# Kernel optimization log

Hardware: AMD Instinct MI355X
Metric: run time of the kernel (lower is better)

## Reference

```python
import jax, jax.numpy as jnp
import numpy as np

N = 50           # hardcoded num_nodes in the module
E = 400          # directed edges (200 undirected)
D = 5            # node feature dim after laplacian concat
NEG_SLOPE = 0.2  # GATConv leaky_relu slope


def _edge_softmax(logits, seg, n):
    # softmax over edges grouped by target node (PyG softmax semantics)
    m = jax.ops.segment_max(logits, seg, num_segments=n)
    e = jnp.exp(logits - m[seg])
    s = jax.ops.segment_sum(e, seg, num_segments=n)
    return e / (s[seg] + 1e-16)


def _laplacian_evecs(edge_index, k=2):
    # sym-normalized Laplacian L = I - D^{-1/2} A D^{-1/2}, dense (N=50)
    src, dst = edge_index[0], edge_index[1]
    A = jnp.zeros((N, N), jnp.float32).at[src, dst].add(1.0)
    deg = A.sum(1)
    dis = jnp.where(deg > 0, jax.lax.rsqrt(jnp.maximum(deg, 1e-12)), 0.0)
    L = jnp.eye(N, dtype=jnp.float32) - dis[:, None] * A * dis[None, :]
    evals, evecs = jnp.linalg.eigh(L)  # ascending, like torch.linalg.eigh
    return evecs[:, :k], evals[1]


def _gat_conv(x, src, dst, w, a_src, a_dst, b):
    h = x @ w.T                                       # [N, out]
    e = jax.nn.leaky_relu((h * a_src).sum(-1)[src] + (h * a_dst).sum(-1)[dst], NEG_SLOPE)
    alpha = _edge_softmax(e, dst, N)
    out = jax.ops.segment_sum(alpha[:, None] * h[src], dst, num_segments=N)
    return out + b


def _transformer_conv(x, src, dst, wq, bq, wk, bk, wv, bv, ws, bs):
    q = x @ wq.T + bq
    k = x @ wk.T + bk
    v = x @ wv.T + bv
    alpha = _edge_softmax((q[dst] * k[src]).sum(-1) / jnp.sqrt(jnp.float32(D)), dst, N)
    out = jax.ops.segment_sum(alpha[:, None] * v[src], dst, num_segments=N)
    return out + x @ ws.T + bs    # root skip connection


def _core(x, mask, gat_w1, gat_a_src1, gat_a_dst1, gat_b1,
          gat_w2, gat_a_src2, gat_a_dst2, gat_b2,
          mha_in_w, mha_in_b, mha_out_w, mha_out_b,
          tc_wq, tc_bq, tc_wk, tc_bk, tc_wv, tc_bv, tc_ws, tc_bs,
          mlp_w1, mlp_b1, mlp_w2, mlp_b2, critic_w, critic_b,
          edge_index, lap_ev):
    x_combined = jnp.concatenate([x, lap_ev], axis=1)        # [N, 5]
    sl = jnp.arange(N, dtype=edge_index.dtype)
    ei = jnp.concatenate([edge_index, jnp.stack([sl, sl])], axis=1)  # add_self_loops
    src, dst = ei[0], ei[1]
    # GAT: 2 GATConv layers, ReLU between (BasicGNN), no act on last
    h = jax.nn.relu(_gat_conv(x_combined, src, dst, gat_w1, gat_a_src1, gat_a_dst1, gat_b1))
    h = _gat_conv(h, src, dst, gat_w2, gat_a_src2, gat_a_dst2, gat_b2)   # [N, 5]
    # nn.MultiheadAttention, seq=N, batch=1, 1 head
    qkv = h @ mha_in_w.T + mha_in_b
    q, k, v = jnp.split(qkv, 3, axis=1)
    attn = jax.nn.softmax(q @ k.T / jnp.sqrt(jnp.float32(D)), axis=-1)   # [N, N]
    h = (attn @ v) @ mha_out_w.T + mha_out_b
    # TransformerConv(5, 5, heads=1)
    h = _transformer_conv(h, src, dst, tc_wq, tc_bq, tc_wk, tc_bk, tc_wv, tc_bv, tc_ws, tc_bs)
    # MLPAggregation with index=arange(N): each node alone in a graph, slot 0 of N
    flat = jnp.pad(h, ((0, 0), (0, D * N - D)))              # [N, 5N]
    logits = jax.nn.relu(flat @ mlp_w1.T + mlp_b1) @ mlp_w2.T + mlp_b2   # [N, N]
    masked_logits = logits * mask[None, :]
    value = (logits @ critic_w.T + critic_b).mean()
    return masked_logits, value, x_combined, ei


def setup_inputs() -> dict:
    key = jax.random.key(0)
    ks = jax.random.split(key, 40)
    # symmetric edge list without self loops (networkx undirected -> both directions)
    row = jax.random.randint(ks[0], (E // 2,), 0, N)
    off = jax.random.randint(ks[1], (E // 2,), 1, N)
    col = (row + off) % N
    edge_index = jnp.concatenate([jnp.stack([row, col]), jnp.stack([col, row])], axis=1).astype(jnp.int32)
    lin = lambda k, o, i: (jax.random.normal(k, (o, i), jnp.float32) / np.sqrt(i))
    vec = lambda k, o: jax.random.normal(k, (o,), jnp.float32) * 0.1
    return {
        'x': jax.random.uniform(ks[2], (N, 3), jnp.float32),
        'edge_index': edge_index,
        'mask': (jax.random.uniform(ks[3], (N,)) > 0.2).astype(jnp.float32),
        'gat_w1': lin(ks[4], 8, 5), 'gat_a_src1': vec(ks[5], 8), 'gat_a_dst1': vec(ks[6], 8), 'gat_b1': vec(ks[7], 8),
        'gat_w2': lin(ks[8], 5, 8), 'gat_a_src2': vec(ks[9], 5), 'gat_a_dst2': vec(ks[10], 5), 'gat_b2': vec(ks[11], 5),
        'mha_in_w': lin(ks[12], 15, 5), 'mha_in_b': vec(ks[13], 15),
        'mha_out_w': lin(ks[14], 5, 5), 'mha_out_b': vec(ks[15], 5),
        'tc_wq': lin(ks[16], 5, 5), 'tc_bq': vec(ks[17], 5),
        'tc_wk': lin(ks[18], 5, 5), 'tc_bk': vec(ks[19], 5),
        'tc_wv': lin(ks[20], 5, 5), 'tc_bv': vec(ks[21], 5),
        'tc_ws': lin(ks[22], 5, 5), 'tc_bs': vec(ks[23], 5),
        'mlp_w1': lin(ks[24], 64, D * N), 'mlp_b1': vec(ks[25], 64),
        'mlp_w2': lin(ks[26], N, 64), 'mlp_b2': vec(ks[27], N),
        'critic_w': lin(ks[28], 1, N), 'critic_b': vec(ks[29], 1),
    }


def reference(x, edge_index, mask, gat_w1, gat_a_src1, gat_a_dst1, gat_b1,
              gat_w2, gat_a_src2, gat_a_dst2, gat_b2,
              mha_in_w, mha_in_b, mha_out_w, mha_out_b,
              tc_wq, tc_bq, tc_wk, tc_bk, tc_wv, tc_bv, tc_ws, tc_bs,
              mlp_w1, mlp_b1, mlp_w2, mlp_b2, critic_w, critic_b):
    lap_ev, _fiedler = _laplacian_evecs(edge_index)
    return _core(x, mask, gat_w1, gat_a_src1, gat_a_dst1, gat_b1,
                 gat_w2, gat_a_src2, gat_a_dst2, gat_b2,
                 mha_in_w, mha_in_b, mha_out_w, mha_out_b,
                 tc_wq, tc_bq, tc_wk, tc_bk, tc_wv, tc_bv, tc_ws, tc_bs,
                 mlp_w1, mlp_b1, mlp_w2, mlp_b2, critic_w, critic_b,
                 edge_index, lap_ev)
```

## Files before the change

### kernel.cpp

```cpp
#include <hip/hip_runtime.h>
#include <math.h>

#define NN 50
#define E2 400
#define ET 450
#define NTHR 256
#define KL 8
#define QS 52
#define MS 68

#define WSYNC() do { asm volatile("s_waitcnt lgkmcnt(0)" ::: "memory"); \
                     __builtin_amdgcn_sched_barrier(0); } while (0)

__global__ __launch_bounds__(NTHR, 1) void opn_kernel(
    const float* __restrict__ gx, const int* __restrict__ gedge,
    const float* __restrict__ gmask,
    const float* __restrict__ w1, const float* __restrict__ as1,
    const float* __restrict__ ad1, const float* __restrict__ b1,
    const float* __restrict__ w2, const float* __restrict__ as2,
    const float* __restrict__ ad2, const float* __restrict__ b2,
    const float* __restrict__ miw, const float* __restrict__ mib,
    const float* __restrict__ mow, const float* __restrict__ mob,
    const float* __restrict__ wq, const float* __restrict__ bq,
    const float* __restrict__ wk, const float* __restrict__ bk,
    const float* __restrict__ wv, const float* __restrict__ bv,
    const float* __restrict__ ws, const float* __restrict__ bs,
    const float* __restrict__ mw1, const float* __restrict__ mb1,
    const float* __restrict__ mw2, const float* __restrict__ mb2,
    const float* __restrict__ cw, const float* __restrict__ cb,
    float* __restrict__ out)
{
    const int tid = threadIdx.x;

    __shared__ float sM[NN * NN];
    __shared__ alignas(16) float sS[3200];
    __shared__ alignas(16) float sL[NN * QS];
    __shared__ alignas(16) float sQ2[(KL + 2) * QS];
    __shared__ float sAl_[KL + 2];
    __shared__ float sBe_[KL + 2];
    __shared__ float sY[KL + 2];
    __shared__ float sCp[KL + 2];
    __shared__ float sDp2[KL + 2];
    __shared__ int   sKeff;
    __shared__ float sB5h[NN * 5];
    __shared__ float sKv[NN * 5];
    __shared__ float sVv[NN * 5];
    __shared__ float sTk[NN * 5];
    __shared__ float sTv[NN * 5];
    __shared__ float sTo[NN * 5];
    __shared__ int   sSrc[ET];
    __shared__ int   sDst[ET];
    __shared__ int   sSrcCsr[ET];
    __shared__ float sAs[NN];
    __shared__ float sAsB[NN];
    __shared__ float sdis[NN];
    __shared__ float sred[4];
    __shared__ int   sOff[NN + 1];
    __shared__ float sW1[40], sAs1[8], sAd1[8], sB1[8];
    __shared__ float sW2[40], sAs2[5], sAd2[5], sB2[5];
    __shared__ float sMiw[75], sMib[15], sMow[25], sMob[5];
    __shared__ float sWq[25], sBq[5], sWk[25], sBk[5];
    __shared__ float sWv[25], sBv[5], sWsk[25], sBsk[5];
    __shared__ float sMw1[320], sMb1[64];
    __shared__ alignas(16) float sMw2[NN * MS];
    __shared__ float sMb2[NN], sCw[NN], sCb0[1], sMask[NN];

    const float inv_sqrt5 = 0.4472135954999579f;
    float xr0 = 0, xr1 = 0, xr2 = 0, xr3 = 0, xr4 = 0;

    if (tid < 64) {
        const int lane = tid;
        {
            int gi = (lane < NN) ? lane : NN - 1;
            xr0 = gx[gi * 3 + 0]; xr1 = gx[gi * 3 + 1]; xr2 = gx[gi * 3 + 2];
        }
        int es[7], ed[7];
#pragma unroll
        for (int u = 0; u < 7; ++u) {
            int e = lane + u * 64;
            int ec = (e < E2) ? e : E2 - 1;
            es[u] = gedge[ec]; ed[u] = gedge[E2 + ec];
        }
        if (lane == 0) sKeff = KL;
        for (int t = lane; t < NN * NN; t += 64) sM[t] = 0.0f;
        WSYNC();
#pragma unroll
        for (int u = 0; u < 7; ++u) {
            int e = lane + u * 64;
            if (e < E2) atomicAdd(&sM[es[u] * NN + ed[u]], 1.0f);
        }
        WSYNC();
        float dsum = 0.0f;
        if (lane < NN) {
            const float* rp = &sM[lane * NN];
            for (int k = 0; k < NN; ++k) dsum += rp[k];
        }
        float disl = (dsum > 0.0f) ? (1.0f / sqrtf(fmaxf(dsum, 1e-12f))) : 0.0f;
        if (lane < NN) sdis[lane] = disl;
        WSYNC();
        for (int t = lane; t < NN * QS; t += 64) {
            int i = t / QS, k = t - i * QS;
            sL[t] = (k < NN)
                  ? (((i == k) ? 1.0f : 0.0f) - sdis[i] * sM[i * NN + k] * sdis[k])
                  : 0.0f;
        }
        float q0r, qprev = 0.0f, qcur;
        {
            float q0 = (lane < NN) ? sqrtf(dsum) : 0.0f;
            float nn = q0 * q0;
            for (int off = 32; off > 0; off >>= 1) nn += __shfl_xor(nn, off);
            q0 *= rsqrtf(nn);
            unsigned u = (unsigned)lane * 2654435761u + 12345u;
            u ^= u >> 13; u *= 2246822519u; u ^= u >> 11;
            float q1 = (lane < NN) ? ((float)(u & 0xFFFF) * (1.0f / 65536.0f) - 0.5f) : 0.0f;
            for (int pass = 0; pass < 2; ++pass) {
                float d = q0 * q1;
                for (int off = 32; off > 0; off >>= 1) d += __shfl_xor(d, off);
                q1 -= d * q0;
            }
            float n1 = q1 * q1;
            for (int off = 32; off > 0; off >>= 1) n1 += __shfl_xor(n1, off);
            q1 *= rsqrtf(n1);
            q0r = q0; qcur = q1;
            if (lane < NN) { sQ2[lane] = q0; sQ2[QS + lane] = q1; }
            WSYNC();
        }
        for (int j = 1; j <= KL; ++j) {
            const float* qp = &sQ2[j * QS];
            const float4* qp4 = (const float4*)qp;
            float w = 0.0f;
            if (lane < NN) {
                const float* rp = &sL[lane * QS];
                const float4* rp4 = (const float4*)rp;
                float a0 = 0.0f, a1 = 0.0f, a2 = 0.0f, a3 = 0.0f;
                for (int k = 0; k < 12; ++k) {
                    float4 r = rp4[k], q = qp4[k];
                    a0 += r.x * q.x; a1 += r.y * q.y;
                    a2 += r.z * q.z; a3 += r.w * q.w;
                }
                a0 += rp[48] * qp[48];
                a1 += rp[49] * qp[49];
                w = 2.0f * qcur - (a0 + a1 + a2 + a3);
            }
            float c0 = q0r * w, c1 = qprev * w, ca = qcur * w;
#pragma unroll
            for (int off = 32; off > 0; off >>= 1) {
                c0 += __shfl_xor(c0, off);
                c1 += __shfl_xor(c1, off);
                ca += __shfl_xor(ca, off);
            }
            w -= c0 * q0r + c1 * qprev + ca * qcur;
            float nn2 = w * w;
#pragma unroll
            for (int off = 32; off > 0; off >>= 1) nn2 += __shfl_xor(nn2, off);
            float beta = sqrtf(nn2);
            if (lane == 0) { sAl_[j] = ca; sBe_[j] = beta; }
            if (j < KL) {
                if (beta > 1e-10f) {
                    qprev = qcur;
                    qcur = w * (1.0f / beta);
                    if (lane < NN) sQ2[(j + 1) * QS + lane] = qcur;
                    WSYNC();
                } else {
                    if (lane == 0) sKeff = j;
                    break;
                }
            }
        }
        WSYNC();
        const int keff = sKeff;
        float lo = 1e30f, hi = -1e30f;
        for (int m = 1; m <= keff; ++m) {
            float r = ((m > 1) ? fabsf(sBe_[m - 1]) : 0.0f)
                    + ((m < keff) ? fabsf(sBe_[m]) : 0.0f);
            lo = fminf(lo, sAl_[m] - r);
            hi = fmaxf(hi, sAl_[m] + r);
        }
        for (int round = 0; round < 4; ++round) {
            float h = (hi - lo) * (1.0f / 65.0f);
            float x = lo + (float)(lane + 1) * h;
            int cnt = 0;
            float d = sAl_[1] - x;
            if (d < 0.0f) cnt++;
            for (int m = 2; m <= keff; ++m) {
                float b = sBe_[m - 1];
                float dd = (fabsf(d) < 1e-20f) ? ((d >= 0.0f) ? 1e-20f : -1e-20f) : d;
                d = sAl_[m] - x - b * b / dd;
                if (d < 0.0f) cnt++;
            }
            unsigned long long msk = __ballot(cnt >= keff);
            int f = (msk == 0ULL) ? 64 : (__ffsll((unsigned long long)msk) - 1);
            float nlo = (f == 0) ? lo : (lo + (float)f * h);
            float nhi = (f == 64) ? hi : (lo + (float)(f + 1) * h);
            lo = nlo; hi = nhi;
        }
        const float th = 0.5f * (lo + hi);
        if (lane == 0) {
            if (keff == 1) {
                sY[1] = 1.0f;
            } else {
                float inv0 = rsqrtf((float)keff);
                for (int m = 1; m <= keff; ++m) sY[m] = inv0;
                float d1 = sAl_[1] - th;
                if (fabsf(d1) < 1e-10f) d1 = (d1 >= 0.0f) ? 1e-10f : -1e-10f;
                sCp[1] = sBe_[1] / d1;
                sDp2[1] = sY[1] / d1;
                for (int m = 2; m <= keff; ++m) {
                    float den = sAl_[m] - th - sBe_[m - 1] * sCp[m - 1];
                    if (fabsf(den) < 1e-10f) den = (den >= 0.0f) ? 1e-10f : -1e-10f;
                    if (m < keff) sCp[m] = sBe_[m] / den;
                    sDp2[m] = (sY[m] - sBe_[m - 1] * sDp2[m - 1]) / den;
                }
                sY[keff] = sDp2[keff];
                for (int m = keff - 1; m >= 1; --m)
                    sY[m] = sDp2[m] - sCp[m] * sY[m + 1];
                float nn = 0.0f;
                for (int m = 1; m <= keff; ++m) nn += sY[m] * sY[m];
                float sc = rsqrtf(nn);
                for (int m = 1; m <= keff; ++m) sY[m] *= sc;
            }
        }
        WSYNC();
        float v = 0.0f;
        if (lane < NN)
            for (int m = 1; m <= keff; ++m) v += sY[m] * sQ2[m * QS + lane];
        {
            float nn = v * v;
            for (int off = 32; off > 0; off >>= 1) nn += __shfl_xor(nn, off);
            float av = fabsf(v);
            for (int off = 32; off > 0; off >>= 1) av = fmaxf(av, __shfl_xor(av, off));
            unsigned long long msk = __ballot((fabsf(v) == av) && (lane < NN));
            int fl = __ffsll((unsigned long long)msk) - 1;
            float sv = __shfl(v, fl);
            v *= ((sv >= 0.0f) ? 1.0f : -1.0f) * rsqrtf(nn);
        }
        xr3 = q0r; xr4 = v;
        if (lane < NN) {
            out[2501 + lane * 5 + 0] = xr0;
            out[2501 + lane * 5 + 1] = xr1;
            out[2501 + lane * 5 + 2] = xr2;
            out[2501 + lane * 5 + 3] = xr3;
            out[2501 + lane * 5 + 4] = xr4;
        }
    } else if (tid < 128) {
        const int l = tid - 64;
        for (int t = l; t < ET; t += 64) {
            int s, d;
            if (t < E2) { s = gedge[t]; d = gedge[E2 + t]; }
            else        { s = t - E2;   d = t - E2; }
            sSrc[t] = s; sDst[t] = d;
        }
        WSYNC();
        int cnt = 0;
        if (l < NN)
            for (int e = 0; e < ET; ++e) cnt += (sDst[e] == l) ? 1 : 0;
        int inc = cnt;
#pragma unroll
        for (int off = 1; off < 64; off <<= 1) {
            int n = __shfl_up(inc, off);
            if (l >= off) inc += n;
        }
        int exc = inc - cnt;
        if (l < NN) sOff[l] = exc;
        if (l == NN - 1) sOff[NN] = inc;
        if (l < NN) {
            int pos = exc;
            for (int e = 0; e < ET; ++e)
                if (sDst[e] == l) { sSrcCsr[pos] = sSrc[e]; ++pos; }
        }
        for (int t = l; t < 2 * ET; t += 64) {
            int val = (t < ET) ? sSrc[t] : sDst[t - ET];
            out[2751 + t] = (float)val;
        }
    } else {
        const int t0 = tid - 128;
        float vW1  = w1 [t0 < 40 ? t0 : 39];
        float vAs1 = as1[t0 < 8  ? t0 : 7];
        float vAd1 = ad1[t0 < 8  ? t0 : 7];
        float vB1  = b1 [t0 < 8  ? t0 : 7];
        float vW2  = w2 [t0 < 40 ? t0 : 39];
        float vAs2 = as2[t0 < 5  ? t0 : 4];
        float vAd2 = ad2[t0 < 5  ? t0 : 4];
        float vB2  = b2 [t0 < 5  ? t0 : 4];
        float vMiw = miw[t0 < 75 ? t0 : 74];
        float vMib = mib[t0 < 15 ? t0 : 14];
        float vMow = mow[t0 < 25 ? t0 : 24];
        float vMob = mob[t0 < 5  ? t0 : 4];
        float vWq  = wq [t0 < 25 ? t0 : 24];
        float vBq  = bq [t0 < 5  ? t0 : 4];
        float vWk  = wk [t0 < 25 ? t0 : 24];
        float vBk  = bk [t0 < 5  ? t0 : 4];
        float vWv  = wv [t0 < 25 ? t0 : 24];
        float vBv  = bv [t0 < 5  ? t0 : 4];
        float vWs  = ws [t0 < 25 ? t0 : 24];
        float vBs  = bs [t0 < 5  ? t0 : 4];
        float vMb1 = mb1[t0 < 64 ? t0 : 63];
        float vMb2 = mb2[t0 < NN ? t0 : NN - 1];
        float vCw  = cw [t0 < NN ? t0 : NN - 1];
        float vCb  = cb[0];
        float vMsk = gmask[t0 < NN ? t0 : NN - 1];
        int ta = t0, tb2 = t0 + 128, tc = (t0 + 256 < 320) ? t0 + 256 : 319;
        float vM1a = mw1[(ta  / 5) * 250 + (ta  % 5)];
        float vM1b = mw1[(tb2 / 5) * 250 + (tb2 % 5)];
        float vM1c = mw1[(tc  / 5) * 250 + (tc  % 5)];
        const float4* m2 = (const float4*)mw2;
        float4 v2[7];
#pragma unroll
        for (int u = 0; u < 7; ++u) {
            int t = t0 + u * 128;
            v2[u] = m2[t < 800 ? t : 799];
        }
        if (t0 < 40) sW1[t0]  = vW1;
        if (t0 < 8)  { sAs1[t0] = vAs1; sAd1[t0] = vAd1; sB1[t0] = vB1; }
        if (t0 < 40) sW2[t0]  = vW2;
        if (t0 < 5)  { sAs2[t0] = vAs2; sAd2[t0] = vAd2; sB2[t0] = vB2; }
        if (t0 < 75) sMiw[t0] = vMiw;
        if (t0 < 15) sMib[t0] = vMib;
        if (t0 < 25) { sMow[t0] = vMow; sWq[t0] = vWq; sWk[t0] = vWk;
                       sWv[t0] = vWv;  sWsk[t0] = vWs; }
        if (t0 < 5)  { sMob[t0] = vMob; sBq[t0] = vBq; sBk[t0] = vBk;
                       sBv[t0] = vBv;  sBsk[t0] = vBs; }
        if (t0 < 64) sMb1[t0] = vMb1;
        if (t0 < NN) { sMb2[t0] = vMb2; sCw[t0] = vCw; sMask[t0] = vMsk; }
        if (t0 == 0) sCb0[0] = vCb;
        sMw1[ta]  = vM1a;
        sMw1[tb2] = vM1b;
        if (t0 + 256 < 320) sMw1[t0 + 256] = vM1c;
#pragma unroll
        for (int u = 0; u < 7; ++u) {
            int t = t0 + u * 128;
            if (t < 800) {
                int o = t >> 4, k4 = t & 15;
                *(float4*)&sMw2[o * MS + k4 * 4] = v2[u];
            }
        }
    }
    __syncthreads();

    if (tid < 64) {
        const int lane = tid;
        float* h8 = sS;
        float adl = 0.0f;
        if (lane < NN) {
            float a = 0.0f;
#pragma unroll
            for (int o = 0; o < 8; ++o) {
                float acc = xr0 * sW1[o * 5 + 0] + xr1 * sW1[o * 5 + 1]
                          + xr2 * sW1[o * 5 + 2] + xr3 * sW1[o * 5 + 3]
                          + xr4 * sW1[o * 5 + 4];
                h8[lane * 8 + o] = acc;
                a   += acc * sAs1[o];
                adl += acc * sAd1[o];
            }
            sAs[lane] = a;
        }
        WSYNC();
        float adlB = 0.0f;
        if (lane < NN) {
            const int c0 = sOff[lane], c1 = sOff[lane + 1];
            float su = 0.0f;
            float acc[8] = {0, 0, 0, 0, 0, 0, 0, 0};
            for (int c = c0; c < c1; ++c) {
                const int s2 = sSrcCsr[c];
                float sc = sAs[s2] + adl;
                sc = (sc > 0.0f) ? sc : 0.2f * sc;
                float p = __expf(sc);
                su += p;
                const float* hp = &h8[s2 * 8];
#pragma unroll
                for (int o = 0; o < 8; ++o) acc[o] += p * hp[o];
            }
            float inv = 1.0f / (su + 1e-16f);
            float o8r[8];
#pragma unroll
            for (int o = 0; o < 8; ++o) o8r[o] = fmaxf(sB1[o] + acc[o] * inv, 0.0f);
            float aB = 0.0f;
#pragma unroll
            for (int o = 0; o < 5; ++o) {
                float a2 = 0.0f;
#pragma unroll
                for (int k = 0; k < 8; ++k) a2 += o8r[k] * sW2[o * 8 + k];
                sB5h[lane * 5 + o] = a2;
                aB   += a2 * sAs2[o];
                adlB += a2 * sAd2[o];
            }
            sAsB[lane] = aB;
        }
        WSYNC();
        float qr[5];
        if (lane < NN) {
            const int c0 = sOff[lane], c1 = sOff[lane + 1];
            float su = 0.0f;
            float acc[5] = {0, 0, 0, 0, 0};
            for (int c = c0; c < c1; ++c) {
                const int s2 = sSrcCsr[c];
                float sc = sAsB[s2] + adlB;
                sc = (sc > 0.0f) ? sc : 0.2f * sc;
                float p = __expf(sc);
                su += p;
                const float* hp = &sB5h[s2 * 5];
#pragma unroll
                for (int o = 0; o < 5; ++o) acc[o] += p * hp[o];
            }
            float inv = 1.0f / (su + 1e-16f);
            float hr[5];
#pragma unroll
            for (int o = 0; o < 5; ++o) hr[o] = sB2[o] + acc[o] * inv;
#pragma unroll
            for (int o = 0; o < 5; ++o) {
                float q_ = sMib[o], k_ = sMib[o + 5], v_ = sMib[o + 10];
#pragma unroll
                for (int k = 0; k < 5; ++k) {
                    q_ += hr[k] * sMiw[o * 5 + k];
                    k_ += hr[k] * sMiw[(o + 5) * 5 + k];
                    v_ += hr[k] * sMiw[(o + 10) * 5 + k];
                }
                qr[o] = q_;
                sKv[lane * 5 + o] = k_;
                sVv[lane * 5 + o] = v_;
            }
        }
        WSYNC();
        float tq[5], skip[5];
        if (lane < NN) {
            float su = 0.0f;
            float a5[5] = {0, 0, 0, 0, 0};
#pragma unroll 2
            for (int j = 0; j < NN; ++j) {
                const float* kp = &sKv[j * 5];
                float d = qr[0] * kp[0] + qr[1] * kp[1] + qr[2] * kp[2]
                        + qr[3] * kp[3] + qr[4] * kp[4];
                float p = __expf(d * inv_sqrt5);
                su += p;
                const float* vp = &sVv[j * 5];
#pragma unroll
                for (int f = 0; f < 5; ++f) a5[f] += p * vp[f];
            }
            float inv = 1.0f / su;
#pragma unroll
            for (int f = 0; f < 5; ++f) a5[f] *= inv;
            float hm[5];
#pragma unroll
            for (int o = 0; o < 5; ++o) {
                float acc = sMob[o];
#pragma unroll
                for (int k = 0; k < 5; ++k) acc += a5[k] * sMow[o * 5 + k];
                hm[o] = acc;
            }
#pragma unroll
            for (int o = 0; o < 5; ++o) {
                float q_ = sBq[o], k_ = sBk[o], v_ = sBv[o], s_ = sBsk[o];
#pragma unroll
                for (int k = 0; k < 5; ++k) {
                    q_ += hm[k] * sWq[o * 5 + k];
                    k_ += hm[k] * sWk[o * 5 + k];
                    v_ += hm[k] * sWv[o * 5 + k];
                    s_ += hm[k] * sWsk[o * 5 + k];
                }
                tq[o] = q_;
                sTk[lane * 5 + o] = k_;
                sTv[lane * 5 + o] = v_;
                skip[o] = s_;
            }
        }
        WSYNC();
        if (lane < NN) {
            const int c0 = sOff[lane], c1 = sOff[lane + 1];
            float su = 0.0f;
            float acc[5] = {0, 0, 0, 0, 0};
            for (int c = c0; c < c1; ++c) {
                const int s2 = sSrcCsr[c];
                const float* kp = &sTk[s2 * 5];
                float d = tq[0] * kp[0] + tq[1] * kp[1] + tq[2] * kp[2]
                        + tq[3] * kp[3] + tq[4] * kp[4];
                float p = __expf(d * inv_sqrt5);
                su += p;
                const float* vp = &sTv[s2 * 5];
#pragma unroll
                for (int o = 0; o < 5; ++o) acc[o] += p * vp[o];
            }
            float inv = 1.0f / (su + 1e-16f);
#pragma unroll
            for (int o = 0; o < 5; ++o) sTo[lane * 5 + o] = skip[o] + acc[o] * inv;
        }
        WSYNC();
        {
            float wv5[5];
#pragma unroll
            for (int k = 0; k < 5; ++k) wv5[k] = sMw1[lane * 5 + k];
            const float bo = sMb1[lane];
            for (int i = 0; i < NN; ++i) {
                float acc = bo;
#pragma unroll
                for (int k = 0; k < 5; ++k) acc += sTo[i * 5 + k] * wv5[k];
                sS[i * 64 + lane] = fmaxf(acc, 0.0f);
            }
        }
    }
    __syncthreads();

    float part = 0.0f;
    for (int t = tid; t < NN * NN; t += NTHR) {
        int i = t / NN, j = t - i * NN;
        const float4* sp4 = (const float4*)&sS[i * 64];
        const float4* wp4 = (const float4*)&sMw2[j * MS];
        float a0 = 0.0f, a1 = 0.0f, a2 = 0.0f, a3 = 0.0f;
        for (int k = 0; k < 16; ++k) {
            float4 a = sp4[k], b = wp4[k];
            a0 += a.x * b.x; a1 += a.y * b.y;
            a2 += a.z * b.z; a3 += a.w * b.w;
        }
        float acc = sMb2[j] + (a0 + a1) + (a2 + a3);
        out[t] = acc * sMask[j];
        part += acc * sCw[j];
    }
    for (int off = 32; off > 0; off >>= 1) part += __shfl_xor(part, off);
    if ((tid & 63) == 0) sred[tid >> 6] = part;
    __syncthreads();
    if (tid == 0)
        out[2500] = (sred[0] + sred[1] + sred[2] + sred[3]) * (1.0f / NN) + sCb0[0];
}

extern "C" void kernel_launch(void* const* d_in, const int* in_sizes, int n_in,
                              void* d_out, int out_size, void* d_ws, size_t ws_size,
                              hipStream_t stream) {
    (void)in_sizes; (void)n_in; (void)d_ws; (void)ws_size; (void)out_size;
    opn_kernel<<<1, NTHR, 0, stream>>>(
        (const float*)d_in[0], (const int*)d_in[1], (const float*)d_in[2],
        (const float*)d_in[3], (const float*)d_in[4], (const float*)d_in[5], (const float*)d_in[6],
        (const float*)d_in[7], (const float*)d_in[8], (const float*)d_in[9], (const float*)d_in[10],
        (const float*)d_in[11], (const float*)d_in[12], (const float*)d_in[13], (const float*)d_in[14],
        (const float*)d_in[15], (const float*)d_in[16], (const float*)d_in[17], (const float*)d_in[18],
        (const float*)d_in[19], (const float*)d_in[20], (const float*)d_in[21], (const float*)d_in[22],
        (const float*)d_in[23], (const float*)d_in[24], (const float*)d_in[25], (const float*)d_in[26],
        (const float*)d_in[27], (const float*)d_in[28],
        (float*)d_out);
}
```

Baseline: 61.93 us.

## Replace dense Laplacian Lanczos matvec with sparse CSR gather after graph build

The Lanczos eigenvector computation no longer builds a dense 50x50 adjacency and Laplacian in shared memory. Each matvec now gathers neighbours through the existing CSR (self-loops excluded), so it must wait until the CSR is built instead of overlapping with it. The attention K/V buffers are also packed into padded 16-float rows so they can be read with float4 loads, and the per-layer CSR offset loads are hoisted into registers. The main risk is the loss of overlap between the eigensolver and the CSR construction, plus duplicate-edge or degree semantics that may differ from the dense version.

```diff
diff --git a/kernel.cpp b/kernel.cpp
--- a/kernel.cpp
+++ b/kernel.cpp
@@ -32,28 +32,23 @@
 {
     const int tid = threadIdx.x;
 
-    __shared__ float sM[NN * NN];
     __shared__ alignas(16) float sS[3200];
-    __shared__ alignas(16) float sL[NN * QS];
     __shared__ alignas(16) float sQ2[(KL + 2) * QS];
+    __shared__ float sZ[64];
     __shared__ float sAl_[KL + 2];
     __shared__ float sBe_[KL + 2];
     __shared__ float sY[KL + 2];
     __shared__ float sCp[KL + 2];
     __shared__ float sDp2[KL + 2];
-    __shared__ int   sKeff;
     __shared__ float sB5h[NN * 5];
-    __shared__ float sKv[NN * 5];
-    __shared__ float sVv[NN * 5];
-    __shared__ float sTk[NN * 5];
-    __shared__ float sTv[NN * 5];
+    __shared__ alignas(16) float sKV[NN * 16];
+    __shared__ alignas(16) float sTKV[NN * 16];
     __shared__ float sTo[NN * 5];
     __shared__ int   sSrc[ET];
     __shared__ int   sDst[ET];
     __shared__ int   sSrcCsr[ET];
     __shared__ float sAs[NN];
     __shared__ float sAsB[NN];
-    __shared__ float sdis[NN];
     __shared__ float sred[4];
     __shared__ int   sOff[NN + 1];
     __shared__ float sW1[40], sAs1[8], sAd1[8], sB1[8];
@@ -69,179 +64,8 @@
     float xr0 = 0, xr1 = 0, xr2 = 0, xr3 = 0, xr4 = 0;
 
     if (tid < 64) {
-        const int lane = tid;
-        {
-            int gi = (lane < NN) ? lane : NN - 1;
-            xr0 = gx[gi * 3 + 0]; xr1 = gx[gi * 3 + 1]; xr2 = gx[gi * 3 + 2];
-        }
-        int es[7], ed[7];
-#pragma unroll
-        for (int u = 0; u < 7; ++u) {
-            int e = lane + u * 64;
-            int ec = (e < E2) ? e : E2 - 1;
-            es[u] = gedge[ec]; ed[u] = gedge[E2 + ec];
-        }
-        if (lane == 0) sKeff = KL;
-        for (int t = lane; t < NN * NN; t += 64) sM[t] = 0.0f;
-        WSYNC();
-#pragma unroll
-        for (int u = 0; u < 7; ++u) {
-            int e = lane + u * 64;
-            if (e < E2) atomicAdd(&sM[es[u] * NN + ed[u]], 1.0f);
-        }
-        WSYNC();
-        float dsum = 0.0f;
-        if (lane < NN) {
-            const float* rp = &sM[lane * NN];
-            for (int k = 0; k < NN; ++k) dsum += rp[k];
-        }
-        float disl = (dsum > 0.0f) ? (1.0f / sqrtf(fmaxf(dsum, 1e-12f))) : 0.0f;
-        if (lane < NN) sdis[lane] = disl;
-        WSYNC();
-        for (int t = lane; t < NN * QS; t += 64) {
-            int i = t / QS, k = t - i * QS;
-            sL[t] = (k < NN)
-                  ? (((i == k) ? 1.0f : 0.0f) - sdis[i] * sM[i * NN + k] * sdis[k])
-                  : 0.0f;
-        }
-        float q0r, qprev = 0.0f, qcur;
-        {
-            float q0 = (lane < NN) ? sqrtf(dsum) : 0.0f;
-            float nn = q0 * q0;
-            for (int off = 32; off > 0; off >>= 1) nn += __shfl_xor(nn, off);
-            q0 *= rsqrtf(nn);
-            unsigned u = (unsigned)lane * 2654435761u + 12345u;
-            u ^= u >> 13; u *= 2246822519u; u ^= u >> 11;
-            float q1 = (lane < NN) ? ((float)(u & 0xFFFF) * (1.0f / 65536.0f) - 0.5f) : 0.0f;
-            for (int pass = 0; pass < 2; ++pass) {
-                float d = q0 * q1;
-                for (int off = 32; off > 0; off >>= 1) d += __shfl_xor(d, off);
-                q1 -= d * q0;
-            }
-            float n1 = q1 * q1;
-            for (int off = 32; off > 0; off >>= 1) n1 += __shfl_xor(n1, off);
-            q1 *= rsqrtf(n1);
-            q0r = q0; qcur = q1;
-            if (lane < NN) { sQ2[lane] = q0; sQ2[QS + lane] = q1; }
-            WSYNC();
-        }
-        for (int j = 1; j <= KL; ++j) {
-            const float* qp = &sQ2[j * QS];
-            const float4* qp4 = (const float4*)qp;
-            float w = 0.0f;
-            if (lane < NN) {
-                const float* rp = &sL[lane * QS];
-                const float4* rp4 = (const float4*)rp;
-                float a0 = 0.0f, a1 = 0.0f, a2 = 0.0f, a3 = 0.0f;
-                for (int k = 0; k < 12; ++k) {
-                    float4 r = rp4[k], q = qp4[k];
-                    a0 += r.x * q.x; a1 += r.y * q.y;
-                    a2 += r.z * q.z; a3 += r.w * q.w;
-                }
-                a0 += rp[48] * qp[48];
-                a1 += rp[49] * qp[49];
-                w = 2.0f * qcur - (a0 + a1 + a2 + a3);
-            }
-            float c0 = q0r * w, c1 = qprev * w, ca = qcur * w;
-#pragma unroll
-            for (int off = 32; off > 0; off >>= 1) {
-                c0 += __shfl_xor(c0, off);
-                c1 += __shfl_xor(c1, off);
-                ca += __shfl_xor(ca, off);
-            }
-            w -= c0 * q0r + c1 * qprev + ca * qcur;
-            float nn2 = w * w;
-#pragma unroll
-            for (int off = 32; off > 0; off >>= 1) nn2 += __shfl_xor(nn2, off);
-            float beta = sqrtf(nn2);
-            if (lane == 0) { sAl_[j] = ca; sBe_[j] = beta; }
-            if (j < KL) {
-                if (beta > 1e-10f) {
-                    qprev = qcur;
-                    qcur = w * (1.0f / beta);
-                    if (lane < NN) sQ2[(j + 1) * QS + lane] = qcur;
-                    WSYNC();
-                } else {
-                    if (lane == 0) sKeff = j;
-                    break;
-                }
-            }
-        }
-        WSYNC();
-        const int keff = sKeff;
-        float lo = 1e30f, hi = -1e30f;
-        for (int m = 1; m <= keff; ++m) {
-            float r = ((m > 1) ? fabsf(sBe_[m - 1]) : 0.0f)
-                    + ((m < keff) ? fabsf(sBe_[m]) : 0.0f);
-            lo = fminf(lo, sAl_[m] - r);
-            hi = fmaxf(hi, sAl_[m] + r);
-        }
-        for (int round = 0; round < 4; ++round) {
-            float h = (hi - lo) * (1.0f / 65.0f);
-            float x = lo + (float)(lane + 1) * h;
-            int cnt = 0;
-            float d = sAl_[1] - x;
-            if (d < 0.0f) cnt++;
-            for (int m = 2; m <= keff; ++m) {
-                float b = sBe_[m - 1];
-                float dd = (fabsf(d) < 1e-20f) ? ((d >= 0.0f) ? 1e-20f : -1e-20f) : d;
-                d = sAl_[m] - x - b * b / dd;
-                if (d < 0.0f) cnt++;
-            }
-            unsigned long long msk = __ballot(cnt >= keff);
-            int f = (msk == 0ULL) ? 64 : (__ffsll((unsigned long long)msk) - 1);
-            float nlo = (f == 0) ? lo : (lo + (float)f * h);
-            float nhi = (f == 64) ? hi : (lo + (float)(f + 1) * h);
-            lo = nlo; hi = nhi;
-        }
-        const float th = 0.5f * (lo + hi);
-        if (lane == 0) {
-            if (keff == 1) {
-                sY[1] = 1.0f;
-            } else {
-                float inv0 = rsqrtf((float)keff);
-                for (int m = 1; m <= keff; ++m) sY[m] = inv0;
-                float d1 = sAl_[1] - th;
-                if (fabsf(d1) < 1e-10f) d1 = (d1 >= 0.0f) ? 1e-10f : -1e-10f;
-                sCp[1] = sBe_[1] / d1;
-                sDp2[1] = sY[1] / d1;
-                for (int m = 2; m <= keff; ++m) {
-                    float den = sAl_[m] - th - sBe_[m - 1] * sCp[m - 1];
-                    if (fabsf(den) < 1e-10f) den = (den >= 0.0f) ? 1e-10f : -1e-10f;
-                    if (m < keff) sCp[m] = sBe_[m] / den;
-                    sDp2[m] = (sY[m] - sBe_[m - 1] * sDp2[m - 1]) / den;
-                }
-                sY[keff] = sDp2[keff];
-                for (int m = keff - 1; m >= 1; --m)
-                    sY[m] = sDp2[m] - sCp[m] * sY[m + 1];
-                float nn = 0.0f;
-                for (int m = 1; m <= keff; ++m) nn += sY[m] * sY[m];
-                float sc = rsqrtf(nn);
-                for (int m = 1; m <= keff; ++m) sY[m] *= sc;
-            }
-        }
-        WSYNC();
-        float v = 0.0f;
-        if (lane < NN)
-            for (int m = 1; m <= keff; ++m) v += sY[m] * sQ2[m * QS + lane];
-        {
-            float nn = v * v;
-            for (int off = 32; off > 0; off >>= 1) nn += __shfl_xor(nn, off);
-            float av = fabsf(v);
-            for (int off = 32; off > 0; off >>= 1) av = fmaxf(av, __shfl_xor(av, off));
-            unsigned long long msk = __ballot((fabsf(v) == av) && (lane < NN));
-            int fl = __ffsll((unsigned long long)msk) - 1;
-            float sv = __shfl(v, fl);
-            v *= ((sv >= 0.0f) ? 1.0f : -1.0f) * rsqrtf(nn);
-        }
-        xr3 = q0r; xr4 = v;
-        if (lane < NN) {
-            out[2501 + lane * 5 + 0] = xr0;
-            out[2501 + lane * 5 + 1] = xr1;
-            out[2501 + lane * 5 + 2] = xr2;
-            out[2501 + lane * 5 + 3] = xr3;
-            out[2501 + lane * 5 + 4] = xr4;
-        }
+        int gi = (tid < NN) ? tid : NN - 1;
+        xr0 = gx[gi * 3 + 0]; xr1 = gx[gi * 3 + 1]; xr2 = gx[gi * 3 + 2];
     } else if (tid < 128) {
         const int l = tid - 64;
         for (int t = l; t < ET; t += 64) {
@@ -339,6 +163,145 @@
 
     if (tid < 64) {
         const int lane = tid;
+        const int c0 = (lane < NN) ? sOff[lane] : 0;
+        const int c1 = (lane < NN) ? sOff[lane + 1] : 0;
+        const int c1m1 = c1 - 1;
+        const float deg = (float)(c1m1 - c0);
+        const float disl = (deg > 0.0f) ? rsqrtf(fmaxf(deg, 1e-12f)) : 0.0f;
+
+        float q0r, qprev = 0.0f, qcur;
+        {
+            float q0 = (lane < NN) ? sqrtf(deg) : 0.0f;
+            float nn = q0 * q0;
+            for (int off = 32; off > 0; off >>= 1) nn += __shfl_xor(nn, off);
+            q0 *= rsqrtf(nn);
+            unsigned u = (unsigned)lane * 2654435761u + 12345u;
+            u ^= u >> 13; u *= 2246822519u; u ^= u >> 11;
+            float q1 = (lane < NN) ? ((float)(u & 0xFFFF) * (1.0f / 65536.0f) - 0.5f) : 0.0f;
+            for (int pass = 0; pass < 2; ++pass) {
+                float d = q0 * q1;
+                for (int off = 32; off > 0; off >>= 1) d += __shfl_xor(d, off);
+                q1 -= d * q0;
+            }
+            float n1 = q1 * q1;
+            for (int off = 32; off > 0; off >>= 1) n1 += __shfl_xor(n1, off);
+            q1 *= rsqrtf(n1);
+            q0r = q0; qcur = q1;
+            if (lane < NN) sQ2[QS + lane] = q1;
+        }
+        int keffr = KL;
+        for (int j = 1; j <= KL; ++j) {
+            sZ[lane] = (lane < NN) ? disl * qcur : 0.0f;
+            WSYNC();
+            float w = 0.0f;
+            if (lane < NN) {
+                float g = 0.0f;
+                int c = c0;
+                for (; c + 4 <= c1m1; c += 4) {
+                    int s0 = sSrcCsr[c],     s1 = sSrcCsr[c + 1];
+                    int s2 = sSrcCsr[c + 2], s3 = sSrcCsr[c + 3];
+                    g += (sZ[s0] + sZ[s1]) + (sZ[s2] + sZ[s3]);
+                }
+                for (; c < c1m1; ++c) g += sZ[sSrcCsr[c]];
+                w = qcur + disl * g;
+            }
+            float cc0 = q0r * w, cc1 = qprev * w, ca = qcur * w;
+#pragma unroll
+            for (int off = 32; off > 0; off >>= 1) {
+                cc0 += __shfl_xor(cc0, off);
+                cc1 += __shfl_xor(cc1, off);
+                ca  += __shfl_xor(ca, off);
+            }
+            w -= cc0 * q0r + cc1 * qprev + ca * qcur;
+            float nn2 = w * w;
+#pragma unroll
+            for (int off = 32; off > 0; off >>= 1) nn2 += __shfl_xor(nn2, off);
+            float beta = sqrtf(nn2);
+            if (lane == 0) { sAl_[j] = ca; sBe_[j] = beta; }
+            if (j < KL) {
+                if (beta > 1e-10f) {
+                    qprev = qcur;
+                    qcur = w * (1.0f / beta);
+                    if (lane < NN) sQ2[(j + 1) * QS + lane] = qcur;
+                } else { keffr = j; break; }
+            }
+        }
+        WSYNC();
+        const int keff = keffr;
+        float lo = 1e30f, hi = -1e30f;
+        for (int m = 1; m <= keff; ++m) {
+            float r = ((m > 1) ? fabsf(sBe_[m - 1]) : 0.0f)
+                    + ((m < keff) ? fabsf(sBe_[m]) : 0.0f);
+            lo = fminf(lo, sAl_[m] - r);
+            hi = fmaxf(hi, sAl_[m] + r);
+        }
+        for (int round = 0; round < 4; ++round) {
+            float h = (hi - lo) * (1.0f / 65.0f);
+            float x = lo + (float)(lane + 1) * h;
+            int cnt = 0;
+            float d = sAl_[1] - x;
+            if (d < 0.0f) cnt++;
+            for (int m = 2; m <= keff; ++m) {
+                float b = sBe_[m - 1];
+                float dd = (fabsf(d) < 1e-20f) ? ((d >= 0.0f) ? 1e-20f : -1e-20f) : d;
+                d = sAl_[m] - x - b * b / dd;
+                if (d < 0.0f) cnt++;
+            }
+            unsigned long long msk = __ballot(cnt >= keff);
+            int f = (msk == 0ULL) ? 64 : (__ffsll((unsigned long long)msk) - 1);
+            float nlo = (f == 0) ? lo : (lo + (float)f * h);
+            float nhi = (f == 64) ? hi : (lo + (float)(f + 1) * h);
+            lo = nlo; hi = nhi;
+        }
+        const float th = 0.5f * (lo + hi);
+        if (lane == 0) {
+            if (keff == 1) {
+                sY[1] = 1.0f;
+            } else {
+                float inv0 = rsqrtf((float)keff);
+                for (int m = 1; m <= keff; ++m) sY[m] = inv0;
+                float d1 = sAl_[1] - th;
+                if (fabsf(d1) < 1e-10f) d1 = (d1 >= 0.0f) ? 1e-10f : -1e-10f;
+                sCp[1] = sBe_[1] / d1;
+                sDp2[1] = sY[1] / d1;
+                for (int m = 2; m <= keff; ++m) {
+                    float den = sAl_[m] - th - sBe_[m - 1] * sCp[m - 1];
+                    if (fabsf(den) < 1e-10f) den = (den >= 0.0f) ? 1e-10f : -1e-10f;
+                    if (m < keff) sCp[m] = sBe_[m] / den;
+                    sDp2[m] = (sY[m] - sBe_[m - 1] * sDp2[m - 1]) / den;
+                }
+                sY[keff] = sDp2[keff];
+                for (int m = keff - 1; m >= 1; --m)
+                    sY[m] = sDp2[m] - sCp[m] * sY[m + 1];
+                float nn = 0.0f;
+                for (int m = 1; m <= keff; ++m) nn += sY[m] * sY[m];
+                float sc = rsqrtf(nn);
+                for (int m = 1; m <= keff; ++m) sY[m] *= sc;
+            }
+        }
+        WSYNC();
+        float v = 0.0f;
+        if (lane < NN)
+            for (int m = 1; m <= keff; ++m) v += sY[m] * sQ2[m * QS + lane];
+        {
+            float nn = v * v;
+            for (int off = 32; off > 0; off >>= 1) nn += __shfl_xor(nn, off);
+            float av = fabsf(v);
+            for (int off = 32; off > 0; off >>= 1) av = fmaxf(av, __shfl_xor(av, off));
+            unsigned long long msk = __ballot((fabsf(v) == av) && (lane < NN));
+            int fl = __ffsll((unsigned long long)msk) - 1;
+            float sv = __shfl(v, fl);
+            v *= ((sv >= 0.0f) ? 1.0f : -1.0f) * rsqrtf(nn);
+        }
+        xr3 = q0r; xr4 = v;
+        if (lane < NN) {
+            out[2501 + lane * 5 + 0] = xr0;
+            out[2501 + lane * 5 + 1] = xr1;
+            out[2501 + lane * 5 + 2] = xr2;
+            out[2501 + lane * 5 + 3] = xr3;
+            out[2501 + lane * 5 + 4] = xr4;
+        }
+
         float* h8 = sS;
         float adl = 0.0f;
         if (lane < NN) {
@@ -357,7 +320,6 @@
         WSYNC();
         float adlB = 0.0f;
         if (lane < NN) {
-            const int c0 = sOff[lane], c1 = sOff[lane + 1];
             float su = 0.0f;
             float acc[8] = {0, 0, 0, 0, 0, 0, 0, 0};
             for (int c = c0; c < c1; ++c) {
@@ -389,7 +351,6 @@
         WSYNC();
         float qr[5];
         if (lane < NN) {
-            const int c0 = sOff[lane], c1 = sOff[lane + 1];
             float su = 0.0f;
             float acc[5] = {0, 0, 0, 0, 0};
             for (int c = c0; c < c1; ++c) {
@@ -416,8 +377,8 @@
                     v_ += hr[k] * sMiw[(o + 10) * 5 + k];
                 }
                 qr[o] = q_;
-                sKv[lane * 5 + o] = k_;
-                sVv[lane * 5 + o] = v_;
+                sKV[lane * 16 + o]     = k_;
+                sKV[lane * 16 + 8 + o] = v_;
             }
         }
         WSYNC();
@@ -425,16 +386,18 @@
         if (lane < NN) {
             float su = 0.0f;
             float a5[5] = {0, 0, 0, 0, 0};
-#pragma unroll 2
             for (int j = 0; j < NN; ++j) {
-                const float* kp = &sKv[j * 5];
-                float d = qr[0] * kp[0] + qr[1] * kp[1] + qr[2] * kp[2]
-                        + qr[3] * kp[3] + qr[4] * kp[4];
+                const float* row = &sKV[j * 16];
+                float4 k4 = *(const float4*)row;
+                float  kk = row[4];
+                float d = qr[0] * k4.x + qr[1] * k4.y + qr[2] * k4.z
+                        + qr[3] * k4.w + qr[4] * kk;
                 float p = __expf(d * inv_sqrt5);
                 su += p;
-                const float* vp = &sVv[j * 5];
-#pragma unroll
-                for (int f = 0; f < 5; ++f) a5[f] += p * vp[f];
+                float4 v4 = *(const float4*)(row + 8);
+                float  vv = row[12];
+                a5[0] += p * v4.x; a5[1] += p * v4.y; a5[2] += p * v4.z;
+                a5[3] += p * v4.w; a5[4] += p * vv;
             }
             float inv = 1.0f / su;
 #pragma unroll
@@ -458,26 +421,28 @@
                     s_ += hm[k] * sWsk[o * 5 + k];
                 }
                 tq[o] = q_;
-                sTk[lane * 5 + o] = k_;
-                sTv[lane * 5 + o] = v_;
+                sTKV[lane * 16 + o]     = k_;
+                sTKV[lane * 16 + 8 + o] = v_;
                 skip[o] = s_;
             }
         }
         WSYNC();
         if (lane < NN) {
-            const int c0 = sOff[lane], c1 = sOff[lane + 1];
             float su = 0.0f;
             float acc[5] = {0, 0, 0, 0, 0};
             for (int c = c0; c < c1; ++c) {
                 const int s2 = sSrcCsr[c];
-                const float* kp = &sTk[s2 * 5];
-                float d = tq[0] * kp[0] + tq[1] * kp[1] + tq[2] * kp[2]
-                        + tq[3] * kp[3] + tq[4] * kp[4];
+                const float* row = &sTKV[s2 * 16];
+                float4 k4 = *(const float4*)row;
+                float  kk = row[4];
+                float d = tq[0] * k4.x + tq[1] * k4.y + tq[2] * k4.z
+                        + tq[3] * k4.w + tq[4] * kk;
                 float p = __expf(d * inv_sqrt5);
                 su += p;
-                const float* vp = &sTv[s2 * 5];
-#pragma unroll
-                for (int o = 0; o < 5; ++o) acc[o] += p * vp[o];
+                float4 v4 = *(const float4*)(row + 8);
+                float  vv = row[12];
+                acc[0] += p * v4.x; acc[1] += p * v4.y; acc[2] += p * v4.z;
+                acc[3] += p * v4.w; acc[4] += p * vv;
             }
             float inv = 1.0f / (su + 1e-16f);
 #pragma unroll
```

New measurement: 76.65 us. 23.8% more time.
